# Kernel tuning notes

Hardware: AMD Instinct MI355X
Metric: run time of the kernel (lower is better)

Reference implementation:

```python
import jax, jax.numpy as jnp
import numpy as np

N, E, IN_DIM, HID, HEADS, LAYERS = 50000, 320000, 128, 128, 4, 2
C = HID // HEADS  # per-head channels = 32
EPS = 1e-5


def _init(key, shape, fan_in):
    return jax.random.normal(key, shape, dtype=jnp.float32) / np.sqrt(fan_in)


def setup_inputs() -> dict:
    key = jax.random.key(0)
    ks = jax.random.split(key, 20)
    x = jax.random.normal(ks[0], (N, IN_DIM), dtype=jnp.float32)
    edge_index = jax.random.randint(ks[1], (2, E), 0, N, dtype=jnp.int64)
    edge_attr = jax.random.uniform(ks[2], (E, 1), dtype=jnp.float32)
    inp = {
        "x": x, "edge_index": edge_index, "edge_attr": edge_attr,
        "W_in": _init(ks[3], (IN_DIM, HID), IN_DIM),
        "b_in": jnp.zeros((HID,), jnp.float32),
        # per-layer TransformerConv params, stacked on leading layer axis
        "Wq": _init(ks[4], (LAYERS, HID, HID), HID),
        "bq": jnp.zeros((LAYERS, HID), jnp.float32),
        "Wk": _init(ks[5], (LAYERS, HID, HID), HID),
        "bk": jnp.zeros((LAYERS, HID), jnp.float32),
        "Wv": _init(ks[6], (LAYERS, HID, HID), HID),
        "bv": jnp.zeros((LAYERS, HID), jnp.float32),
        "We": _init(ks[7], (LAYERS, 1, HID), 1),          # lin_edge, bias=False
        "Wskip": _init(ks[8], (LAYERS, HID, HID), HID),   # root/skip projection
        "bskip": jnp.zeros((LAYERS, HID), jnp.float32),
        "Wbeta": _init(ks[9], (LAYERS, 3 * HID, 1), 3 * HID),  # lin_beta, bias=False
        "bn_gamma": jnp.ones((LAYERS, HID), jnp.float32),
        "bn_beta": jnp.zeros((LAYERS, HID), jnp.float32),
    }
    return inp


def _transformer_conv(h, src, tgt, edge_attr, Wq, bq, Wk, bk, Wv, bv, We, Wskip, bskip, Wbeta):
    n = h.shape[0]
    q = (h @ Wq + bq).reshape(n, HEADS, C)
    k = (h @ Wk + bk).reshape(n, HEADS, C)
    v = (h @ Wv + bv).reshape(n, HEADS, C)
    e = (edge_attr @ We).reshape(-1, HEADS, C)          # [E,H,C] edge embedding
    k_j = k[src] + e                                     # gather source keys
    alpha = jnp.einsum('ehc,ehc->eh', q[tgt], k_j) / jnp.sqrt(jnp.float32(C))
    amax = jax.ops.segment_max(alpha, tgt, num_segments=n)   # softmax over in-edges per target
    ex = jnp.exp(alpha - amax[tgt])
    denom = jax.ops.segment_sum(ex, tgt, num_segments=n)
    a = ex / denom[tgt]                                  # [E,H]
    msg = (v[src] + e) * a[..., None]
    out = jax.ops.segment_sum(msg, tgt, num_segments=n).reshape(n, HID)
    x_r = h @ Wskip + bskip                              # root weight
    beta = jax.nn.sigmoid(jnp.concatenate([out, x_r, out - x_r], axis=-1) @ Wbeta)
    return beta * x_r + (1.0 - beta) * out


def _batchnorm(h, gamma, beta):
    mu = h.mean(axis=0)
    var = h.var(axis=0)
    return gamma * (h - mu) * jax.lax.rsqrt(var + EPS) + beta


def reference(x, edge_index, edge_attr, W_in, b_in, Wq, bq, Wk, bk, Wv, bv, We, Wskip, bskip, Wbeta, bn_gamma, bn_beta):
    src, tgt = edge_index[0], edge_index[1]
    h = jax.nn.relu(x @ W_in + b_in)
    for l in range(LAYERS):
        h_res = h
        h = _transformer_conv(h, src, tgt, edge_attr, Wq[l], bq[l], Wk[l], bk[l], Wv[l], bv[l], We[l], Wskip[l], bskip[l], Wbeta[l])
        h = jax.nn.relu(_batchnorm(h, bn_gamma[l], bn_beta[l]))
        h = h + h_res
    return h
```

## Files before the change

kernel.cpp:

```cpp
#include <hip/hip_runtime.h>
#include <hip/hip_bf16.h>
#include <math.h>

#define EPS 1e-5f

typedef __attribute__((ext_vector_type(8))) short bf16x8;
typedef __attribute__((ext_vector_type(4))) float f32x4;

__device__ __forceinline__ unsigned short f2bf(float f) {
    unsigned u = __float_as_uint(f);
    unsigned r = (u + 0x7FFFu + ((u >> 16) & 1u)) >> 16;
    return (unsigned short)r;
}
__device__ __forceinline__ unsigned f2bf2(float lo, float hi) {
    return (unsigned)f2bf(lo) | ((unsigned)f2bf(hi) << 16);
}
__device__ __forceinline__ float bf2f(unsigned short u) {
    return __uint_as_float((unsigned)u << 16);
}
__device__ __forceinline__ void bfu2(unsigned u, float& lo, float& hi) {
    lo = __uint_as_float(u << 16);
    hi = __uint_as_float(u & 0xFFFF0000u);
}

__global__ __launch_bounds__(256) void pack_w9(const float* __restrict__ W0, const float* __restrict__ W1,
                                               const float* __restrict__ W2, const float* __restrict__ W3,
                                               const float* __restrict__ W4, const float* __restrict__ W5,
                                               const float* __restrict__ W6, const float* __restrict__ W7,
                                               const float* __restrict__ W8, unsigned short* __restrict__ out) {
    int t = blockIdx.x * 256 + threadIdx.x;
    if (t >= 9 * 16384) return;
    int mat = t >> 14, r = t & 16383;
    const float* W;
    switch (mat) {
        case 0: W = W0; break; case 1: W = W1; break; case 2: W = W2; break;
        case 3: W = W3; break; case 4: W = W4; break; case 5: W = W5; break;
        case 6: W = W6; break; case 7: W = W7; break; default: W = W8; break;
    }
    int j = r & 7, lane = (r >> 3) & 63, nt = (r >> 9) & 7, kc = r >> 12;
    int k = kc * 32 + (lane >> 4) * 8 + j;
    int n = (lane & 15) * 8 + nt;
    out[t] = f2bf(W[k * 128 + n]);
}

__global__ __launch_bounds__(256) void f32_to_bf16(const float* __restrict__ in,
                                                   unsigned short* __restrict__ out, int n4) {
    int i = blockIdx.x * 256 + threadIdx.x;
    if (i >= n4) return;
    float4 v = ((const float4*)in)[i];
    ushort4 o = make_ushort4(f2bf(v.x), f2bf(v.y), f2bf(v.z), f2bf(v.w));
    ((ushort4*)out)[i] = o;
}

template <int ACT, int WBF>
__global__ __launch_bounds__(256) void gemm_mfma(const unsigned short* __restrict__ Abf,
                                                 const unsigned short* __restrict__ Bp,
                                                 const float* __restrict__ bias,
                                                 float* __restrict__ C,
                                                 unsigned short* __restrict__ Cbf, int M) {
    int wave = threadIdx.x >> 6, lane = threadIdx.x & 63;
    int base = blockIdx.x * 64 + wave * 16;
    int m = lane & 15, kg = lane >> 4;
    int arow = base + m; if (arow >= M) arow = M - 1;
    const unsigned short* Aptr = Abf + (size_t)arow * 128 + kg * 8;
    f32x4 acc[8];
#pragma unroll
    for (int nt = 0; nt < 8; ++nt) acc[nt] = (f32x4)(0.f);
#pragma unroll
    for (int kc = 0; kc < 4; ++kc) {
        bf16x8 a = *(const bf16x8*)(Aptr + kc * 32);
        const unsigned short* bp = Bp + (size_t)kc * 4096 + (size_t)lane * 8;
#pragma unroll
        for (int nt = 0; nt < 8; ++nt) {
            bf16x8 b = *(const bf16x8*)(bp + nt * 512);
            acc[nt] = __builtin_amdgcn_mfma_f32_16x16x32_bf16(a, b, acc[nt], 0, 0, 0);
        }
    }
    int col0 = lane & 15;
    int r0 = base + (lane >> 4) * 4;
    float4 bl = *(const float4*)&bias[col0 * 8];
    float4 bh = *(const float4*)&bias[col0 * 8 + 4];
#pragma unroll
    for (int r = 0; r < 4; ++r) {
        int ro = r0 + r;
        if (ro < M) {
            float v0 = acc[0][r] + bl.x, v1 = acc[1][r] + bl.y;
            float v2 = acc[2][r] + bl.z, v3 = acc[3][r] + bl.w;
            float v4 = acc[4][r] + bh.x, v5 = acc[5][r] + bh.y;
            float v6 = acc[6][r] + bh.z, v7 = acc[7][r] + bh.w;
            if (ACT) {
                v0 = fmaxf(v0, 0.f); v1 = fmaxf(v1, 0.f); v2 = fmaxf(v2, 0.f); v3 = fmaxf(v3, 0.f);
                v4 = fmaxf(v4, 0.f); v5 = fmaxf(v5, 0.f); v6 = fmaxf(v6, 0.f); v7 = fmaxf(v7, 0.f);
            }
            size_t o = (size_t)ro * 128 + col0 * 8;
            *(float4*)&C[o]     = make_float4(v0, v1, v2, v3);
            *(float4*)&C[o + 4] = make_float4(v4, v5, v6, v7);
            if (WBF)
                *(uint4*)&Cbf[o] = make_uint4(f2bf2(v0, v1), f2bf2(v2, v3),
                                              f2bf2(v4, v5), f2bf2(v6, v7));
        }
    }
}

__global__ __launch_bounds__(256) void gemm_qk(const unsigned short* __restrict__ Abf,
                                               const unsigned short* __restrict__ Bq,
                                               const unsigned short* __restrict__ Bk,
                                               const float* __restrict__ bq,
                                               const float* __restrict__ bk,
                                               unsigned short* __restrict__ qbf,
                                               unsigned short* __restrict__ kvbf, int M) {
    int wave = threadIdx.x >> 6, lane = threadIdx.x & 63;
    int base = blockIdx.x * 64 + wave * 16;
    int m = lane & 15, kg = lane >> 4;
    int arow = base + m; if (arow >= M) arow = M - 1;
    const unsigned short* Aptr = Abf + (size_t)arow * 128 + kg * 8;
    f32x4 aq[8], ak[8];
#pragma unroll
    for (int nt = 0; nt < 8; ++nt) { aq[nt] = (f32x4)(0.f); ak[nt] = (f32x4)(0.f); }
#pragma unroll
    for (int kc = 0; kc < 4; ++kc) {
        bf16x8 a = *(const bf16x8*)(Aptr + kc * 32);
        size_t boff = (size_t)kc * 4096 + (size_t)lane * 8;
#pragma unroll
        for (int nt = 0; nt < 8; ++nt) {
            bf16x8 b0 = *(const bf16x8*)(Bq + boff + nt * 512);
            aq[nt] = __builtin_amdgcn_mfma_f32_16x16x32_bf16(a, b0, aq[nt], 0, 0, 0);
            bf16x8 b1 = *(const bf16x8*)(Bk + boff + nt * 512);
            ak[nt] = __builtin_amdgcn_mfma_f32_16x16x32_bf16(a, b1, ak[nt], 0, 0, 0);
        }
    }
    int col0 = lane & 15;
    int r0 = base + (lane >> 4) * 4;
    float4 bql = *(const float4*)&bq[col0 * 8], bqh = *(const float4*)&bq[col0 * 8 + 4];
    float4 bkl = *(const float4*)&bk[col0 * 8], bkh = *(const float4*)&bk[col0 * 8 + 4];
#pragma unroll
    for (int r = 0; r < 4; ++r) {
        int ro = r0 + r;
        if (ro < M) {
            size_t qo = (size_t)ro * 128 + col0 * 8;
            size_t kvo = (size_t)ro * 256 + col0 * 8;
            *(uint4*)&qbf[qo] = make_uint4(
                f2bf2(aq[0][r] + bql.x, aq[1][r] + bql.y), f2bf2(aq[2][r] + bql.z, aq[3][r] + bql.w),
                f2bf2(aq[4][r] + bqh.x, aq[5][r] + bqh.y), f2bf2(aq[6][r] + bqh.z, aq[7][r] + bqh.w));
            *(uint4*)&kvbf[kvo] = make_uint4(
                f2bf2(ak[0][r] + bkl.x, ak[1][r] + bkl.y), f2bf2(ak[2][r] + bkl.z, ak[3][r] + bkl.w),
                f2bf2(ak[4][r] + bkh.x, ak[5][r] + bkh.y), f2bf2(ak[6][r] + bkh.z, ak[7][r] + bkh.w));
        }
    }
}

__global__ __launch_bounds__(256) void gemm_vs(const unsigned short* __restrict__ Abf,
                                               const unsigned short* __restrict__ Bv,
                                               const unsigned short* __restrict__ Bs,
                                               const float* __restrict__ bv,
                                               const float* __restrict__ bs,
                                               unsigned short* __restrict__ kvbf,
                                               float* __restrict__ xr, int M) {
    int wave = threadIdx.x >> 6, lane = threadIdx.x & 63;
    int base = blockIdx.x * 64 + wave * 16;
    int m = lane & 15, kg = lane >> 4;
    int arow = base + m; if (arow >= M) arow = M - 1;
    const unsigned short* Aptr = Abf + (size_t)arow * 128 + kg * 8;
    f32x4 av[8], as_[8];
#pragma unroll
    for (int nt = 0; nt < 8; ++nt) { av[nt] = (f32x4)(0.f); as_[nt] = (f32x4)(0.f); }
#pragma unroll
    for (int kc = 0; kc < 4; ++kc) {
        bf16x8 a = *(const bf16x8*)(Aptr + kc * 32);
        size_t boff = (size_t)kc * 4096 + (size_t)lane * 8;
#pragma unroll
        for (int nt = 0; nt < 8; ++nt) {
            bf16x8 b2 = *(const bf16x8*)(Bv + boff + nt * 512);
            av[nt] = __builtin_amdgcn_mfma_f32_16x16x32_bf16(a, b2, av[nt], 0, 0, 0);
            bf16x8 b3 = *(const bf16x8*)(Bs + boff + nt * 512);
            as_[nt] = __builtin_amdgcn_mfma_f32_16x16x32_bf16(a, b3, as_[nt], 0, 0, 0);
        }
    }
    int col0 = lane & 15;
    int r0 = base + (lane >> 4) * 4;
    float4 bvl = *(const float4*)&bv[col0 * 8], bvh = *(const float4*)&bv[col0 * 8 + 4];
    float4 bsl = *(const float4*)&bs[col0 * 8], bsh = *(const float4*)&bs[col0 * 8 + 4];
#pragma unroll
    for (int r = 0; r < 4; ++r) {
        int ro = r0 + r;
        if (ro < M) {
            size_t qo = (size_t)ro * 128 + col0 * 8;
            size_t kvo = (size_t)ro * 256 + 128 + col0 * 8;
            *(uint4*)&kvbf[kvo] = make_uint4(
                f2bf2(av[0][r] + bvl.x, av[1][r] + bvl.y), f2bf2(av[2][r] + bvl.z, av[3][r] + bvl.w),
                f2bf2(av[4][r] + bvh.x, av[5][r] + bvh.y), f2bf2(av[6][r] + bvh.z, av[7][r] + bvh.w));
            *(float4*)&xr[qo]     = make_float4(as_[0][r] + bsl.x, as_[1][r] + bsl.y,
                                                as_[2][r] + bsl.z, as_[3][r] + bsl.w);
            *(float4*)&xr[qo + 4] = make_float4(as_[4][r] + bsh.x, as_[5][r] + bsh.y,
                                                as_[6][r] + bsh.z, as_[7][r] + bsh.w);
        }
    }
}

__global__ __launch_bounds__(256) void csr_hist(const int* __restrict__ ei,
                                                int* __restrict__ deg, int E) {
    int e = blockIdx.x * 256 + threadIdx.x;
    if (e < E) atomicAdd(&deg[ei[E + e]], 1);
}

__global__ __launch_bounds__(256) void scan_block_sums(const int* __restrict__ deg,
                                                       int* __restrict__ bsums, int N) {
    __shared__ int sd[256];
    int i = blockIdx.x * 256 + threadIdx.x;
    sd[threadIdx.x] = (i < N) ? deg[i] : 0;
    __syncthreads();
    for (int off = 128; off > 0; off >>= 1) {
        if (threadIdx.x < off) sd[threadIdx.x] += sd[threadIdx.x + off];
        __syncthreads();
    }
    if (threadIdx.x == 0) bsums[blockIdx.x] = sd[0];
}

__global__ __launch_bounds__(256) void scan_bsums(const int* __restrict__ bsums,
                                                  int* __restrict__ boff, int nb) {
    __shared__ int sd[256];
    int tid = threadIdx.x;
    int per = (nb + 255) / 256;
    int start = tid * per;
    int s = 0;
    for (int i = 0; i < per; ++i) {
        int idx = start + i;
        if (idx < nb) s += bsums[idx];
    }
    int my = s;
    sd[tid] = s;
    __syncthreads();
    for (int off = 1; off < 256; off <<= 1) {
        int t = (tid >= off) ? sd[tid - off] : 0;
        __syncthreads();
        sd[tid] += t;
        __syncthreads();
    }
    int run = sd[tid] - my;
    for (int i = 0; i < per; ++i) {
        int idx = start + i;
        if (idx < nb) {
            boff[idx] = run;
            run += bsums[idx];
        }
    }
}

__global__ __launch_bounds__(256) void scan_local(const int* __restrict__ deg,
                                                  const int* __restrict__ boff,
                                                  int* __restrict__ rowptr,
                                                  int* __restrict__ wrptr, int N, int E) {
    __shared__ int sd[256];
    int i = blockIdx.x * 256 + threadIdx.x;
    int v = (i < N) ? deg[i] : 0;
    sd[threadIdx.x] = v;
    __syncthreads();
    for (int off = 1; off < 256; off <<= 1) {
        int t = (threadIdx.x >= off) ? sd[threadIdx.x - off] : 0;
        __syncthreads();
        sd[threadIdx.x] += t;
        __syncthreads();
    }
    if (i < N) {
        int excl = sd[threadIdx.x] - v + boff[blockIdx.x];
        rowptr[i] = excl;
        wrptr[i] = excl;
        if (i == N - 1) rowptr[N] = E;
    }
}

__global__ __launch_bounds__(256) void csr_fill(const int* __restrict__ ei,
                                                const float* __restrict__ ea,
                                                int* __restrict__ wrptr,
                                                int* __restrict__ csr_src,
                                                float* __restrict__ csr_w, int E) {
    int e = blockIdx.x * 256 + threadIdx.x;
    if (e >= E) return;
    int tgt = ei[E + e];
    int pos = atomicAdd(&wrptr[tgt], 1);
    csr_src[pos] = ei[e];
    csr_w[pos] = ea[e];
}

__global__ __launch_bounds__(256) void attn_gather(const unsigned short* __restrict__ qbf,
                                                   const unsigned short* __restrict__ kvbf,
                                                   const float* __restrict__ xr,
                                                   const int* __restrict__ rowptr,
                                                   const int* __restrict__ csr_src,
                                                   const float* __restrict__ csr_w,
                                                   const float* __restrict__ Wel,
                                                   const float* __restrict__ Wb,
                                                   float* __restrict__ out,
                                                   float* __restrict__ bsumR,
                                                   float* __restrict__ bsumsqR, int N) {
    __shared__ float sdS[4][128];
    __shared__ float sdQ[4][128];
    int tid = threadIdx.x;
    int n = blockIdx.x * 16 + (tid >> 4);
    int sl = tid & 15;
    int wave = tid >> 6, lane = tid & 63;
    bool live = (n < N);
    int nn = live ? n : (N - 1);

    uint4 qu = ((const uint4*)(qbf + (size_t)nn * 128))[sl];
    float qf[8];
    bfu2(qu.x, qf[0], qf[1]); bfu2(qu.y, qf[2], qf[3]);
    bfu2(qu.z, qf[4], qf[5]); bfu2(qu.w, qf[6], qf[7]);
    float wef[8];
    {
        float4 w0 = ((const float4*)Wel)[sl * 2];
        float4 w1 = ((const float4*)Wel)[sl * 2 + 1];
        wef[0] = w0.x; wef[1] = w0.y; wef[2] = w0.z; wef[3] = w0.w;
        wef[4] = w1.x; wef[5] = w1.y; wef[6] = w1.z; wef[7] = w1.w;
    }
    float qwe = 0.f;
#pragma unroll
    for (int c = 0; c < 8; ++c) qwe += qf[c] * wef[c];
    qwe += __shfl_xor(qwe, 1);
    qwe += __shfl_xor(qwe, 2);

    float l = 0.f;
    float acc[8];
#pragma unroll
    for (int c = 0; c < 8; ++c) acc[c] = 0.f;

    int beg = live ? rowptr[nn] : 0;
    int end = live ? rowptr[nn + 1] : 0;
    int i = beg;
    if (i < end) {
        float w = csr_w[i];
        const uint4* kvr = (const uint4*)(kvbf + (size_t)csr_src[i] * 256);
        uint4 ku = kvr[sl];
        uint4 vu = kvr[16 + sl];
        for (;;) {
            float wc = w;
            uint4 kuc = ku, vuc = vu;
            ++i;
            bool more = (i < end);
            if (more) {
                float w2 = csr_w[i];
                const uint4* kvr2 = (const uint4*)(kvbf + (size_t)csr_src[i] * 256);
                ku = kvr2[sl];
                vu = kvr2[16 + sl];
                w = w2;
            }
            float kf[8];
            bfu2(kuc.x, kf[0], kf[1]); bfu2(kuc.y, kf[2], kf[3]);
            bfu2(kuc.z, kf[4], kf[5]); bfu2(kuc.w, kf[6], kf[7]);
            float d = 0.f;
#pragma unroll
            for (int c = 0; c < 8; ++c) d += qf[c] * kf[c];
            d += __shfl_xor(d, 1);
            d += __shfl_xor(d, 2);
            float p = __expf((d + wc * qwe) * 0.17677669529663687f);
            l += p;
            float vf[8];
            bfu2(vuc.x, vf[0], vf[1]); bfu2(vuc.y, vf[2], vf[3]);
            bfu2(vuc.z, vf[4], vf[5]); bfu2(vuc.w, vf[6], vf[7]);
#pragma unroll
            for (int c = 0; c < 8; ++c)
                acc[c] += p * (vf[c] + wc * wef[c]);
            if (!more) break;
        }
    }

    float inv = (l > 0.f) ? 1.f / l : 0.f;
    float ox[8];
#pragma unroll
    for (int c = 0; c < 8; ++c) ox[c] = acc[c] * inv;

    const float* xrow = xr + (size_t)nn * 128;
    float4 a0 = ((const float4*)xrow)[sl * 2];
    float4 a1 = ((const float4*)xrow)[sl * 2 + 1];
    float xv[8] = {a0.x, a0.y, a0.z, a0.w, a1.x, a1.y, a1.z, a1.w};
    float4 b0 = ((const float4*)Wb)[sl * 2];
    float4 b1 = ((const float4*)Wb)[sl * 2 + 1];
    float4 c0 = ((const float4*)(Wb + 128))[sl * 2];
    float4 c1 = ((const float4*)(Wb + 128))[sl * 2 + 1];
    float4 d0 = ((const float4*)(Wb + 256))[sl * 2];
    float4 d1 = ((const float4*)(Wb + 256))[sl * 2 + 1];
    float wb0[8] = {b0.x, b0.y, b0.z, b0.w, b1.x, b1.y, b1.z, b1.w};
    float wb1[8] = {c0.x, c0.y, c0.z, c0.w, c1.x, c1.y, c1.z, c1.w};
    float wb2[8] = {d0.x, d0.y, d0.z, d0.w, d1.x, d1.y, d1.z, d1.w};
    float part = 0.f;
#pragma unroll
    for (int c = 0; c < 8; ++c)
        part += ox[c] * wb0[c] + xv[c] * wb1[c] + (ox[c] - xv[c]) * wb2[c];
    part += __shfl_xor(part, 1); part += __shfl_xor(part, 2);
    part += __shfl_xor(part, 4); part += __shfl_xor(part, 8);
    float beta = 1.f / (1.f + __expf(-part));

    float r[8];
#pragma unroll
    for (int c = 0; c < 8; ++c)
        r[c] = beta * xv[c] + (1.f - beta) * ox[c];

    if (live) {
        ((float4*)(out + (size_t)n * 128))[sl * 2] =
            make_float4(r[0], r[1], r[2], r[3]);
        ((float4*)(out + (size_t)n * 128))[sl * 2 + 1] =
            make_float4(r[4], r[5], r[6], r[7]);
    }

    float s8[8], q8[8];
#pragma unroll
    for (int c = 0; c < 8; ++c) {
        s8[c] = live ? r[c] : 0.f;
        q8[c] = live ? r[c] * r[c] : 0.f;
    }
#pragma unroll
    for (int c = 0; c < 8; ++c) {
        s8[c] += __shfl_xor(s8[c], 16); s8[c] += __shfl_xor(s8[c], 32);
        q8[c] += __shfl_xor(q8[c], 16); q8[c] += __shfl_xor(q8[c], 32);
    }
    if ((lane >> 4) == 0) {
#pragma unroll
        for (int c = 0; c < 8; ++c) {
            sdS[wave][sl * 8 + c] = s8[c];
            sdQ[wave][sl * 8 + c] = q8[c];
        }
    }
    __syncthreads();
    if (tid < 128) {
        float s = sdS[0][tid] + sdS[1][tid] + sdS[2][tid] + sdS[3][tid];
        float q = sdQ[0][tid] + sdQ[1][tid] + sdQ[2][tid] + sdQ[3][tid];
        int rep = blockIdx.x & 7;
        atomicAdd(&bsumR[rep * 128 + tid], s);
        atomicAdd(&bsumsqR[rep * 128 + tid], q);
    }
}

__global__ __launch_bounds__(256) void bn_apply(const float* __restrict__ o,
                                                const float* __restrict__ hres,
                                                float* __restrict__ hout,
                                                unsigned short* __restrict__ hout_bf,
                                                const float* __restrict__ bsumR,
                                                const float* __restrict__ bsumsqR,
                                                const float* __restrict__ gamma,
                                                const float* __restrict__ bbeta,
                                                int N, float invN) {
    int i = blockIdx.x * 256 + threadIdx.x;
    if (i >= N * 32) return;
    int c4 = i & 31;
    float4 s = make_float4(0.f, 0.f, 0.f, 0.f), ss = s;
#pragma unroll
    for (int rep = 0; rep < 8; ++rep) {
        float4 sv = ((const float4*)bsumR)[rep * 32 + c4];
        float4 qv = ((const float4*)bsumsqR)[rep * 32 + c4];
        s.x += sv.x; s.y += sv.y; s.z += sv.z; s.w += sv.w;
        ss.x += qv.x; ss.y += qv.y; ss.z += qv.z; ss.w += qv.w;
    }
    float4 g = ((const float4*)gamma)[c4];
    float4 b = ((const float4*)bbeta)[c4];
    float4 ov = ((const float4*)o)[i];
    float4 hr = ((const float4*)hres)[i];
    float4 r;
    { float mu = s.x * invN, var = ss.x * invN - mu * mu;
      r.x = fmaxf((ov.x - mu) * (g.x * rsqrtf(var + EPS)) + b.x, 0.f) + hr.x; }
    { float mu = s.y * invN, var = ss.y * invN - mu * mu;
      r.y = fmaxf((ov.y - mu) * (g.y * rsqrtf(var + EPS)) + b.y, 0.f) + hr.y; }
    { float mu = s.z * invN, var = ss.z * invN - mu * mu;
      r.z = fmaxf((ov.z - mu) * (g.z * rsqrtf(var + EPS)) + b.z, 0.f) + hr.z; }
    { float mu = s.w * invN, var = ss.w * invN - mu * mu;
      r.w = fmaxf((ov.w - mu) * (g.w * rsqrtf(var + EPS)) + b.w, 0.f) + hr.w; }
    ((float4*)hout)[i] = r;
    if (hout_bf) {
        ushort4 ob = make_ushort4(f2bf(r.x), f2bf(r.y), f2bf(r.z), f2bf(r.w));
        ((ushort4*)hout_bf)[i] = ob;
    }
}

extern "C" void kernel_launch(void* const* d_in, const int* in_sizes, int n_in,
                              void* d_out, int out_size, void* d_ws, size_t ws_size,
                              hipStream_t stream) {
    const float* x     = (const float*)d_in[0];
    const int*   ei    = (const int*)d_in[1];
    const float* ea    = (const float*)d_in[2];
    const float* W_in  = (const float*)d_in[3];
    const float* b_in  = (const float*)d_in[4];
    const float* Wq    = (const float*)d_in[5];
    const float* bq    = (const float*)d_in[6];
    const float* Wk    = (const float*)d_in[7];
    const float* bk    = (const float*)d_in[8];
    const float* Wv    = (const float*)d_in[9];
    const float* bv    = (const float*)d_in[10];
    const float* We    = (const float*)d_in[11];
    const float* Wskip = (const float*)d_in[12];
    const float* bskip = (const float*)d_in[13];
    const float* Wbeta = (const float*)d_in[14];
    const float* bn_g  = (const float*)d_in[15];
    const float* bn_b  = (const float*)d_in[16];

    const int N = in_sizes[0] / 128;
    const int E = in_sizes[1] / 2;

    float* ws = (float*)d_ws;
    unsigned short* Bpack = (unsigned short*)ws;
    size_t off = 73728;
    unsigned short* xbf  = (unsigned short*)(ws + off);               off += (size_t)N * 64;
    unsigned short* hbf  = (unsigned short*)(ws + off);               off += (size_t)N * 64;
    unsigned short* qbf  = (unsigned short*)(ws + off);               off += (size_t)N * 64;
    unsigned short* kvbf = (unsigned short*)(ws + off);               off += (size_t)N * 128;
    float* h    = ws + off;  off += (size_t)N * 128;
    float* xr   = ws + off;  off += (size_t)N * 128;
    float* attn = ws + off;  off += (size_t)N * 128;
    float* bsumR   = ws + off;  off += 1024;
    float* bsumsqR = ws + off;  off += 1024;
    float* csr_w   = ws + off;  off += (size_t)E;
    int* deg     = (int*)(ws + off);
    int* rowptr  = deg + N;
    int* wrptr   = rowptr + (N + 1);
    int* csr_src = wrptr + N;
    int* bsums   = csr_src + E;
    int* boff    = bsums + ((N + 255) / 256 + 1);

    dim3 blk(256);
    int gGemm   = (N + 63) / 64;
    int gNode16 = (N + 15) / 16;
    int gEdge   = (E + 255) / 256;
    int gApply  = (N * 32 + 255) / 256;
    int nbScan  = (N + 255) / 256;

    pack_w9<<<(9 * 16384 + 255) / 256, blk, 0, stream>>>(
        W_in, Wq, Wk, Wv, Wskip, Wq + 16384, Wk + 16384, Wv + 16384, Wskip + 16384, Bpack);
    f32_to_bf16<<<gApply, blk, 0, stream>>>(x, xbf, N * 32);

    hipMemsetAsync(deg, 0, (size_t)N * sizeof(int), stream);
    csr_hist<<<gEdge, blk, 0, stream>>>(ei, deg, E);
    scan_block_sums<<<nbScan, blk, 0, stream>>>(deg, bsums, N);
    scan_bsums<<<1, blk, 0, stream>>>(bsums, boff, nbScan);
    scan_local<<<nbScan, blk, 0, stream>>>(deg, boff, rowptr, wrptr, N, E);
    csr_fill<<<gEdge, blk, 0, stream>>>(ei, ea, wrptr, csr_src, csr_w, E);

    gemm_mfma<1, 1><<<gGemm, blk, 0, stream>>>(xbf, Bpack + 0 * 16384, b_in, h, hbf, N);

    for (int l = 0; l < 2; ++l) {
        const unsigned short* Bq = Bpack + (size_t)(1 + l * 4 + 0) * 16384;
        const unsigned short* Bk = Bpack + (size_t)(1 + l * 4 + 1) * 16384;
        const unsigned short* Bv = Bpack + (size_t)(1 + l * 4 + 2) * 16384;
        const unsigned short* Bs = Bpack + (size_t)(1 + l * 4 + 3) * 16384;
        gemm_qk<<<gGemm, blk, 0, stream>>>(hbf, Bq, Bk, bq + l * 128, bk + l * 128,
                                           qbf, kvbf, N);
        gemm_vs<<<gGemm, blk, 0, stream>>>(hbf, Bv, Bs, bv + l * 128, bskip + l * 128,
                                           kvbf, xr, N);
        hipMemsetAsync(bsumR, 0, 2048 * sizeof(float), stream);
        attn_gather<<<gNode16, blk, 0, stream>>>(qbf, kvbf, xr, rowptr, csr_src, csr_w,
                                                 We + l * 128, Wbeta + l * 384, attn,
                                                 bsumR, bsumsqR, N);
        bn_apply<<<gApply, blk, 0, stream>>>(attn, h, (l == 1) ? (float*)d_out : h,
                                             (l == 0) ? hbf : (unsigned short*)0,
                                             bsumR, bsumsqR, bn_g + l * 128, bn_b + l * 128,
                                             N, 1.0f / (float)N);
    }
}
```

Measured before the change: 345.4 us.

## Interleave CSR src/weight and deepen edge gather prefetch in attention

Packs the CSR source index and edge weight into one int2 array, so each edge needs one 8-byte load instead of two separate loads. The attention gather loop now processes two edges per iteration and keeps K/V rows for two further edges plus the index pairs for two more in flight. This deeper software pipelining is meant to hide the latency of the random K/V row gathers. It raises register pressure and does a wasted clamped load when a node has an odd in-degree.

```diff
diff --git a/kernel.cpp b/kernel.cpp
--- a/kernel.cpp
+++ b/kernel.cpp
@@ -272,22 +272,19 @@
 __global__ __launch_bounds__(256) void csr_fill(const int* __restrict__ ei,
                                                 const float* __restrict__ ea,
                                                 int* __restrict__ wrptr,
-                                                int* __restrict__ csr_src,
-                                                float* __restrict__ csr_w, int E) {
+                                                int2* __restrict__ csr_sw, int E) {
     int e = blockIdx.x * 256 + threadIdx.x;
     if (e >= E) return;
     int tgt = ei[E + e];
     int pos = atomicAdd(&wrptr[tgt], 1);
-    csr_src[pos] = ei[e];
-    csr_w[pos] = ea[e];
+    csr_sw[pos] = make_int2(ei[e], __float_as_int(ea[e]));
 }
 
 __global__ __launch_bounds__(256) void attn_gather(const unsigned short* __restrict__ qbf,
                                                    const unsigned short* __restrict__ kvbf,
                                                    const float* __restrict__ xr,
                                                    const int* __restrict__ rowptr,
-                                                   const int* __restrict__ csr_src,
-                                                   const float* __restrict__ csr_w,
+                                                   const int2* __restrict__ csr_sw,
                                                    const float* __restrict__ Wel,
                                                    const float* __restrict__ Wb,
                                                    float* __restrict__ out,
@@ -326,41 +323,66 @@
 
     int beg = live ? rowptr[nn] : 0;
     int end = live ? rowptr[nn + 1] : 0;
-    int i = beg;
-    if (i < end) {
-        float w = csr_w[i];
-        const uint4* kvr = (const uint4*)(kvbf + (size_t)csr_src[i] * 256);
-        uint4 ku = kvr[sl];
-        uint4 vu = kvr[16 + sl];
-        for (;;) {
-            float wc = w;
-            uint4 kuc = ku, vuc = vu;
-            ++i;
-            bool more = (i < end);
-            if (more) {
-                float w2 = csr_w[i];
-                const uint4* kvr2 = (const uint4*)(kvbf + (size_t)csr_src[i] * 256);
-                ku = kvr2[sl];
-                vu = kvr2[16 + sl];
-                w = w2;
+
+    if (beg < end) {
+        int j1 = (beg + 1 < end) ? beg + 1 : beg;
+        int j2 = (beg + 2 < end) ? beg + 2 : beg;
+        int j3 = (beg + 3 < end) ? beg + 3 : beg;
+        int2 swA = csr_sw[beg], swB = csr_sw[j1];
+        int2 swC = csr_sw[j2], swD = csr_sw[j3];
+        const uint4* rA = (const uint4*)(kvbf + (size_t)swA.x * 256);
+        uint4 ku0 = rA[sl], vu0 = rA[16 + sl];
+        const uint4* rB = (const uint4*)(kvbf + (size_t)swB.x * 256);
+        uint4 ku1 = rB[sl], vu1 = rB[16 + sl];
+
+        for (int i = beg; i < end; i += 2) {
+            const uint4* rC = (const uint4*)(kvbf + (size_t)swC.x * 256);
+            uint4 ku2 = rC[sl], vu2 = rC[16 + sl];
+            const uint4* rD = (const uint4*)(kvbf + (size_t)swD.x * 256);
+            uint4 ku3 = rD[sl], vu3 = rD[16 + sl];
+            int j4 = (i + 4 < end) ? i + 4 : beg;
+            int j5 = (i + 5 < end) ? i + 5 : beg;
+            int2 swE = csr_sw[j4], swF = csr_sw[j5];
+
+            {
+                float w = __int_as_float(swA.y);
+                float kf[8];
+                bfu2(ku0.x, kf[0], kf[1]); bfu2(ku0.y, kf[2], kf[3]);
+                bfu2(ku0.z, kf[4], kf[5]); bfu2(ku0.w, kf[6], kf[7]);
+                float d = 0.f;
+#pragma unroll
+                for (int c = 0; c < 8; ++c) d += qf[c] * kf[c];
+                d += __shfl_xor(d, 1); d += __shfl_xor(d, 2);
+                float p = __expf((d + w * qwe) * 0.17677669529663687f);
+                l += p;
+                float vf[8];
+                bfu2(vu0.x, vf[0], vf[1]); bfu2(vu0.y, vf[2], vf[3]);
+                bfu2(vu0.z, vf[4], vf[5]); bfu2(vu0.w, vf[6], vf[7]);
+#pragma unroll
+                for (int c = 0; c < 8; ++c)
+                    acc[c] += p * (vf[c] + w * wef[c]);
             }
-            float kf[8];
-            bfu2(kuc.x, kf[0], kf[1]); bfu2(kuc.y, kf[2], kf[3]);
-            bfu2(kuc.z, kf[4], kf[5]); bfu2(kuc.w, kf[6], kf[7]);
-            float d = 0.f;
-#pragma unroll
-            for (int c = 0; c < 8; ++c) d += qf[c] * kf[c];
-            d += __shfl_xor(d, 1);
-            d += __shfl_xor(d, 2);
-            float p = __expf((d + wc * qwe) * 0.17677669529663687f);
-            l += p;
-            float vf[8];
-            bfu2(vuc.x, vf[0], vf[1]); bfu2(vuc.y, vf[2], vf[3]);
-            bfu2(vuc.z, vf[4], vf[5]); bfu2(vuc.w, vf[6], vf[7]);
-#pragma unroll
-            for (int c = 0; c < 8; ++c)
-                acc[c] += p * (vf[c] + wc * wef[c]);
-            if (!more) break;
+            {
+                float w = __int_as_float(swB.y);
+                float kf[8];
+                bfu2(ku1.x, kf[0], kf[1]); bfu2(ku1.y, kf[2], kf[3]);
+                bfu2(ku1.z, kf[4], kf[5]); bfu2(ku1.w, kf[6], kf[7]);
+                float d = 0.f;
+#pragma unroll
+                for (int c = 0; c < 8; ++c) d += qf[c] * kf[c];
+                d += __shfl_xor(d, 1); d += __shfl_xor(d, 2);
+                float p = __expf((d + w * qwe) * 0.17677669529663687f);
+                if (i + 1 >= end) p = 0.f;
+                l += p;
+                float vf[8];
+                bfu2(vu1.x, vf[0], vf[1]); bfu2(vu1.y, vf[2], vf[3]);
+                bfu2(vu1.z, vf[4], vf[5]); bfu2(vu1.w, vf[6], vf[7]);
+#pragma unroll
+                for (int c = 0; c < 8; ++c)
+                    acc[c] += p * (vf[c] + w * wef[c]);
+            }
+            swA = swC; swB = swD; swC = swE; swD = swF;
+            ku0 = ku2; vu0 = vu2; ku1 = ku3; vu1 = vu3;
         }
     }
 
@@ -506,12 +528,11 @@
     float* attn = ws + off;  off += (size_t)N * 128;
     float* bsumR   = ws + off;  off += 1024;
     float* bsumsqR = ws + off;  off += 1024;
-    float* csr_w   = ws + off;  off += (size_t)E;
+    int2* csr_sw = (int2*)(ws + off);  off += (size_t)E * 2;
     int* deg     = (int*)(ws + off);
     int* rowptr  = deg + N;
     int* wrptr   = rowptr + (N + 1);
-    int* csr_src = wrptr + N;
-    int* bsums   = csr_src + E;
+    int* bsums   = wrptr + N;
     int* boff    = bsums + ((N + 255) / 256 + 1);
 
     dim3 blk(256);
@@ -530,7 +551,7 @@
     scan_block_sums<<<nbScan, blk, 0, stream>>>(deg, bsums, N);
     scan_bsums<<<1, blk, 0, stream>>>(bsums, boff, nbScan);
     scan_local<<<nbScan, blk, 0, stream>>>(deg, boff, rowptr, wrptr, N, E);
-    csr_fill<<<gEdge, blk, 0, stream>>>(ei, ea, wrptr, csr_src, csr_w, E);
+    csr_fill<<<gEdge, blk, 0, stream>>>(ei, ea, wrptr, csr_sw, E);
 
     gemm_mfma<1, 1><<<gGemm, blk, 0, stream>>>(xbf, Bpack + 0 * 16384, b_in, h, hbf, N);
 
@@ -544,7 +565,7 @@
         gemm_vs<<<gGemm, blk, 0, stream>>>(hbf, Bv, Bs, bv + l * 128, bskip + l * 128,
                                            kvbf, xr, N);
         hipMemsetAsync(bsumR, 0, 2048 * sizeof(float), stream);
-        attn_gather<<<gNode16, blk, 0, stream>>>(qbf, kvbf, xr, rowptr, csr_src, csr_w,
+        attn_gather<<<gNode16, blk, 0, stream>>>(qbf, kvbf, xr, rowptr, csr_sw,
                                                  We + l * 128, Wbeta + l * 384, attn,
                                                  bsumR, bsumsqR, N);
         bn_apply<<<gApply, blk, 0, stream>>>(attn, h, (l == 1) ? (float*)d_out : h,
```

Result: no change. 350.7 us (+1.6%).
